# Kernel optimization log

Measured on AMD Instinct MI355X. Metric: run time of the kernel, lower is better.

Reference implementation:

```python
import jax, jax.numpy as jnp
import numpy as np

N, OBS, H, M, L = 512, 32, 128, 128, 3


def _w(key, shape, fan_in):
    return jax.random.normal(key, shape, dtype=jnp.float32) / np.sqrt(fan_in)


def setup_inputs() -> dict:
    key = jax.random.key(0)
    ks = iter(jax.random.split(key, 64))
    inp = {}
    inp["obs"] = jax.random.normal(next(ks), (N, OBS), dtype=jnp.float32)
    inp["pos"] = jax.random.uniform(next(ks), (N, 2), dtype=jnp.float32)
    # encoder: obs_dim -> H -> H -> H
    inp["enc_W1"] = _w(next(ks), (H, OBS), OBS); inp["enc_b1"] = jnp.zeros((H,), jnp.float32)
    inp["enc_W2"] = _w(next(ks), (H, H), H);     inp["enc_b2"] = jnp.zeros((H,), jnp.float32)
    inp["enc_W3"] = _w(next(ks), (H, H), H);     inp["enc_b3"] = jnp.zeros((H,), jnp.float32)
    # per-layer message MLPs: (2H+1) -> M -> M -> M, stacked over L layers
    inp["msg_W1"] = _w(next(ks), (L, M, 2 * H + 1), 2 * H + 1); inp["msg_b1"] = jnp.zeros((L, M), jnp.float32)
    inp["msg_W2"] = _w(next(ks), (L, M, M), M);                 inp["msg_b2"] = jnp.zeros((L, M), jnp.float32)
    inp["msg_W3"] = _w(next(ks), (L, M, M), M);                 inp["msg_b3"] = jnp.zeros((L, M), jnp.float32)
    # per-layer update MLPs: (H+M) -> H -> H -> H, stacked over L layers
    inp["upd_W1"] = _w(next(ks), (L, H, H + M), H + M); inp["upd_b1"] = jnp.zeros((L, H), jnp.float32)
    inp["upd_W2"] = _w(next(ks), (L, H, H), H);         inp["upd_b2"] = jnp.zeros((L, H), jnp.float32)
    inp["upd_W3"] = _w(next(ks), (L, H, H), H);         inp["upd_b3"] = jnp.zeros((L, H), jnp.float32)
    return inp


def _mlp3(x, W1, b1, W2, b2, W3, b3):
    h = jax.nn.relu(x @ W1.T + b1)
    h = jax.nn.relu(h @ W2.T + b2)
    return h @ W3.T + b3


def reference(obs, pos, enc_W1, enc_b1, enc_W2, enc_b2, enc_W3, enc_b3,
              msg_W1, msg_b1, msg_W2, msg_b2, msg_W3, msg_b3,
              upd_W1, upd_b1, upd_W2, upd_b2, upd_W3, upd_b3):
    n = obs.shape[0]
    h = enc_W1.shape[0]
    z = _mlp3(obs, enc_W1, enc_b1, enc_W2, enc_b2, enc_W3, enc_b3)  # (N, H)
    # pairwise distances; guard diagonal sqrt(0) for grad safety, then zero it
    diff = pos[:, None, :] - pos[None, :, :]                  # (N, N, 2)
    sq = jnp.sum(diff * diff, axis=-1)                        # (N, N)
    eye = jnp.eye(n, dtype=pos.dtype)
    dist = jnp.sqrt(jnp.where(eye > 0, 1.0, sq)) * (1.0 - eye)
    nondiag = (1.0 - eye)[:, :, None]
    n_layers = msg_W1.shape[0]
    for l in range(n_layers):
        W1 = msg_W1[l]
        Wi, Wj, wd = W1[:, :h], W1[:, h:2 * h], W1[:, 2 * h]  # split concat [z_i, z_j, d]
        A = z @ Wi.T                                          # (N, M) receiver term
        B = z @ Wj.T                                          # (N, M) sender term
        h1 = jax.nn.relu(A[:, None, :] + B[None, :, :] + dist[:, :, None] * wd + msg_b1[l])  # (N, N, M)
        h2 = jax.nn.relu(jnp.einsum('ijm,km->ijk', h1, msg_W2[l]) + msg_b2[l])
        m = jnp.einsum('ijm,km->ijk', h2, msg_W3[l]) + msg_b3[l]
        m = m * nondiag                                       # exclude j == i
        msum = jnp.sum(m, axis=1)                             # (N, M) sum over senders j
        z = _mlp3(jnp.concatenate([z, msum], axis=-1),
                  upd_W1[l], upd_b1[l], upd_W2[l], upd_b2[l], upd_W3[l], upd_b3[l])
    return z
```

## Files before the change

kernel.cpp:

```cpp
#include <hip/hip_runtime.h>

#define NA 512
#define NOBS 32
#define NH 128

typedef const float* fp32p;
typedef __attribute__((ext_vector_type(8))) short bf16x8;
typedef __attribute__((ext_vector_type(4))) float f32x4;

__device__ __forceinline__ unsigned cvt_pk_bf16(float lo, float hi) {
    unsigned r;
    asm("v_cvt_pk_bf16_f32 %0, %1, %2" : "=v"(r) : "v"(lo), "v"(hi));
    return r;
}

__device__ __forceinline__ bf16x8 wfrag_f4(const float* p) {
    float4 u = *(const float4*)p;
    float4 v = *(const float4*)(p + 4);
    union { unsigned w[4]; bf16x8 f; } r;
    r.w[0] = cvt_pk_bf16(u.x, u.y);
    r.w[1] = cvt_pk_bf16(u.z, u.w);
    r.w[2] = cvt_pk_bf16(v.x, v.y);
    r.w[3] = cvt_pk_bf16(v.z, v.w);
    return r.f;
}

__device__ __forceinline__ bf16x8 wfrag_s(const float* p) {
    union { unsigned w[4]; bf16x8 f; } r;
    r.w[0] = cvt_pk_bf16(p[0], p[1]);
    r.w[1] = cvt_pk_bf16(p[2], p[3]);
    r.w[2] = cvt_pk_bf16(p[4], p[5]);
    r.w[3] = cvt_pk_bf16(p[6], p[7]);
    return r.f;
}

#define HSTR 136

__global__ __launch_bounds__(512) void enc_ab_kernel(
    fp32p obs, fp32p eW1, fp32p eb1, fp32p eW2, fp32p eb2, fp32p eW3, fp32p eb3,
    fp32p mW1, float* __restrict__ z, float* __restrict__ A, float* __restrict__ B) {
    const int i0 = blockIdx.x * 16;
    const int t = threadIdx.x;
    const int lane = t & 63;
    const int w = t >> 6;
    const int q = lane >> 4;
    const int c = lane & 15;
    const int q8 = q * 8;
    const int ncol = w * 16 + c;

    __shared__ short ha[16 * HSTR];
    __shared__ short hb[16 * HSTR];

    {
        const bf16x8 af = wfrag_f4(obs + (size_t)(i0 + c) * NOBS + q8);
        const bf16x8 bf = wfrag_f4(eW1 + (size_t)ncol * NOBS + q8);
        f32x4 acc = {0.f, 0.f, 0.f, 0.f};
        acc = __builtin_amdgcn_mfma_f32_16x16x32_bf16(af, bf, acc, 0, 0, 0);
        const float bn = eb1[ncol];
        #pragma unroll
        for (int r = 0; r < 4; ++r) {
            const float v = fmaxf(acc[r] + bn, 0.f);
            ha[(q * 4 + r) * HSTR + ncol] = (short)cvt_pk_bf16(v, v);
        }
    }
    __syncthreads();
    {
        f32x4 acc = {0.f, 0.f, 0.f, 0.f};
        const short* ar = &ha[c * HSTR + q8];
        #pragma unroll
        for (int kb = 0; kb < 4; ++kb) {
            const bf16x8 a = *(const bf16x8*)(ar + kb * 32);
            const bf16x8 b = wfrag_f4(eW2 + (size_t)ncol * NH + kb * 32 + q8);
            acc = __builtin_amdgcn_mfma_f32_16x16x32_bf16(a, b, acc, 0, 0, 0);
        }
        const float bn = eb2[ncol];
        #pragma unroll
        for (int r = 0; r < 4; ++r) {
            const float v = fmaxf(acc[r] + bn, 0.f);
            hb[(q * 4 + r) * HSTR + ncol] = (short)cvt_pk_bf16(v, v);
        }
    }
    __syncthreads();
    {
        f32x4 acc = {0.f, 0.f, 0.f, 0.f};
        const short* ar = &hb[c * HSTR + q8];
        #pragma unroll
        for (int kb = 0; kb < 4; ++kb) {
            const bf16x8 a = *(const bf16x8*)(ar + kb * 32);
            const bf16x8 b = wfrag_f4(eW3 + (size_t)ncol * NH + kb * 32 + q8);
            acc = __builtin_amdgcn_mfma_f32_16x16x32_bf16(a, b, acc, 0, 0, 0);
        }
        const float bn = eb3[ncol];
        #pragma unroll
        for (int r = 0; r < 4; ++r) {
            const float v = acc[r] + bn;
            z[(size_t)(i0 + q * 4 + r) * NH + ncol] = v;
            ha[(q * 4 + r) * HSTR + ncol] = (short)cvt_pk_bf16(v, v);
        }
    }
    __syncthreads();
    {
        f32x4 aa = {0.f, 0.f, 0.f, 0.f};
        f32x4 ab = {0.f, 0.f, 0.f, 0.f};
        const short* ar = &ha[c * HSTR + q8];
        const float* wrow = mW1 + (size_t)ncol * 257;
        #pragma unroll
        for (int kb = 0; kb < 4; ++kb) {
            const bf16x8 a = *(const bf16x8*)(ar + kb * 32);
            const bf16x8 bi = wfrag_s(wrow + kb * 32 + q8);
            const bf16x8 bj = wfrag_s(wrow + 128 + kb * 32 + q8);
            aa = __builtin_amdgcn_mfma_f32_16x16x32_bf16(a, bi, aa, 0, 0, 0);
            ab = __builtin_amdgcn_mfma_f32_16x16x32_bf16(a, bj, ab, 0, 0, 0);
        }
        #pragma unroll
        for (int r = 0; r < 4; ++r) {
            A[(size_t)(i0 + q * 4 + r) * NH + ncol] = aa[r];
            B[(size_t)(i0 + q * 4 + r) * NH + ncol] = ab[r];
        }
    }
}

__global__ __launch_bounds__(512) void msg_upd_kernel(
    const float* __restrict__ A, const float* __restrict__ B,
    fp32p pos, const float* __restrict__ zin,
    fp32p W1l, fp32p b1, fp32p W2, fp32p b2, fp32p W3, fp32p b3,
    fp32p uW1, fp32p ub1, fp32p uW2, fp32p ub2, fp32p uW3, fp32p ub3,
    fp32p msgW1n, int do_ab,
    float* __restrict__ zout, float* __restrict__ An, float* __restrict__ Bn) {
    const int i = blockIdx.x;
    const int t = threadIdx.x;
    const int lane = t & 63;
    const int w = t >> 6;
    const int q = lane >> 4;
    const int c = lane & 15;
    const int ncol = w * 16 + c;

    __shared__ short h1s[128 * HSTR];
    __shared__ short h2s[128 * HSTR];
    __shared__ float distrow[NA];
    __shared__ float amrow[NH];
    __shared__ float wdsr[NH];
    __shared__ float xs2[2 * NH];
    __shared__ float part[4 * NH];
    __shared__ float part2[4 * NH];
    __shared__ float hx[NH], hy[NH], hz[NH];

    if (t < NH) {
        amrow[t] = A[i * NH + t] + b1[t];
        wdsr[t]  = W1l[t * 257 + 256];
        xs2[t] = zin[(size_t)i * NH + t];
    }
    {
        const float2 pi = *(const float2*)&pos[2 * i];
        const float2 pj = *(const float2*)&pos[2 * t];
        const float dx = pi.x - pj.x, dy = pi.y - pj.y;
        const float s = dx * dx + dy * dy;
        distrow[t] = (t == i) ? 0.0f : sqrtf(s);
    }

    bf16x8 w2f[4], w3f[4];
    {
        const float* w2r = W2 + (size_t)ncol * NH + q * 8;
        const float* w3r = W3 + (size_t)ncol * NH + q * 8;
        #pragma unroll
        for (int kb = 0; kb < 4; ++kb) {
            w2f[kb] = wfrag_f4(w2r + kb * 32);
            w3f[kb] = wfrag_f4(w3r + kb * 32);
        }
    }
    const float b2n = b2[ncol];

    const int m2 = lane * 2;
    float psum = 0.0f;

    __syncthreads();
    const float am0 = amrow[m2], am1 = amrow[m2 + 1];
    const float wd0 = wdsr[m2],  wd1 = wdsr[m2 + 1];

#define BUILD(c4_) do {                                                      \
        const int j0_ = (c4_) * 128;                                         \
        _Pragma("unroll")                                                    \
        for (int rr = 0; rr < 16; ++rr) {                                    \
            const int row_ = rr * 8 + w;                                     \
            const int jg_ = j0_ + row_;                                      \
            const float2 bv_ = *(const float2*)&B[(size_t)jg_ * NH + m2];    \
            const float d_ = distrow[jg_];                                   \
            const float v0_ = fmaxf(fmaf(d_, wd0, am0 + bv_.x), 0.0f);       \
            const float v1_ = fmaxf(fmaf(d_, wd1, am1 + bv_.y), 0.0f);       \
            *(unsigned*)&h1s[row_ * HSTR + m2] = cvt_pk_bf16(v0_, v1_);      \
        }                                                                    \
    } while (0)

#define GEMM1() do {                                                         \
        _Pragma("unroll")                                                    \
        for (int jt = 0; jt < 8; ++jt) {                                     \
            f32x4 acc = {0.f, 0.f, 0.f, 0.f};                                \
            const short* arow = &h1s[(jt * 16 + c) * HSTR + q * 8];          \
            _Pragma("unroll")                                                \
            for (int kb = 0; kb < 4; ++kb) {                                 \
                bf16x8 a = *(const bf16x8*)(arow + kb * 32);                 \
                acc = __builtin_amdgcn_mfma_f32_16x16x32_bf16(a, w2f[kb], acc, 0, 0, 0); \
            }                                                                \
            const int orow = jt * 16 + q * 4;                                \
            const unsigned p01 = cvt_pk_bf16(fmaxf(acc[0] + b2n, 0.0f),      \
                                             fmaxf(acc[1] + b2n, 0.0f));     \
            const unsigned p23 = cvt_pk_bf16(fmaxf(acc[2] + b2n, 0.0f),      \
                                             fmaxf(acc[3] + b2n, 0.0f));     \
            const unsigned send = (c & 1) ? p01 : p23;                       \
            const unsigned recv = __shfl_xor(send, 1, 64);                   \
            const unsigned keep = (c & 1) ? p23 : p01;                       \
            const unsigned lo = (c & 1) ? recv : keep;                       \
            const unsigned hi = (c & 1) ? keep : recv;                       \
            const unsigned d0 = (lo & 0xFFFFu) | (hi << 16);                 \
            const unsigned d1 = (lo >> 16) | (hi & 0xFFFF0000u);             \
            const int rbase = orow + ((c & 1) << 1);                         \
            const int colb = ncol & ~1;                                      \
            *(unsigned*)&h2s[(rbase + 0) * HSTR + colb] = d0;                \
            *(unsigned*)&h2s[(rbase + 1) * HSTR + colb] = d1;                \
        }                                                                    \
    } while (0)

#define GEMM2(c4_) do {                                                      \
        const int j0_ = (c4_) * 128;                                         \
        _Pragma("unroll")                                                    \
        for (int jt = 0; jt < 8; ++jt) {                                     \
            f32x4 acc = {0.f, 0.f, 0.f, 0.f};                                \
            const short* arow = &h2s[(jt * 16 + c) * HSTR + q * 8];          \
            _Pragma("unroll")                                                \
            for (int kb = 0; kb < 4; ++kb) {                                 \
                bf16x8 a = *(const bf16x8*)(arow + kb * 32);                 \
                acc = __builtin_amdgcn_mfma_f32_16x16x32_bf16(a, w3f[kb], acc, 0, 0, 0); \
            }                                                                \
            _Pragma("unroll")                                                \
            for (int r = 0; r < 4; ++r) {                                    \
                const int jg_ = j0_ + jt * 16 + q * 4 + r;                   \
                if (jg_ != i) psum += acc[r];                                \
            }                                                                \
        }                                                                    \
    } while (0)

    BUILD(0);
    __syncthreads();
    GEMM1();
    for (int c4 = 0; c4 < 4; ++c4) {
        __syncthreads();
        if (c4 < 3) {
            BUILD(c4 + 1);
            GEMM2(c4);
            __syncthreads();
            GEMM1();
        } else {
            GEMM2(c4);
        }
    }
#undef BUILD
#undef GEMM1
#undef GEMM2

    psum += __shfl_xor(psum, 16, 64);
    psum += __shfl_xor(psum, 32, 64);
    if (lane < 16) xs2[NH + ncol] = psum + 511.0f * b3[ncol];
    __syncthreads();

    const int nn = t >> 2;
    const int ks = t & 3;
    {
        const float* wr = uW1 + (size_t)nn * 256 + ks * 4;
        float p = 0.f;
        #pragma unroll
        for (int it = 0; it < 16; ++it) {
            const float4 wv = *(const float4*)(wr + it * 16);
            const float4 xv = *(const float4*)&xs2[it * 16 + ks * 4];
            p += wv.x * xv.x + wv.y * xv.y + wv.z * xv.z + wv.w * xv.w;
        }
        part[ks * NH + nn] = p;
    }
    __syncthreads();
    if (t < NH)
        hx[t] = fmaxf(ub1[t] + part[t] + part[NH + t] + part[2 * NH + t] + part[3 * NH + t], 0.f);
    __syncthreads();
    {
        const float* wr = uW2 + (size_t)nn * NH + ks * 4;
        float p = 0.f;
        #pragma unroll
        for (int it = 0; it < 8; ++it) {
            const float4 wv = *(const float4*)(wr + it * 16);
            const float4 xv = *(const float4*)&hx[it * 16 + ks * 4];
            p += wv.x * xv.x + wv.y * xv.y + wv.z * xv.z + wv.w * xv.w;
        }
        part[ks * NH + nn] = p;
    }
    __syncthreads();
    if (t < NH)
        hy[t] = fmaxf(ub2[t] + part[t] + part[NH + t] + part[2 * NH + t] + part[3 * NH + t], 0.f);
    __syncthreads();
    {
        const float* wr = uW3 + (size_t)nn * NH + ks * 4;
        float p = 0.f;
        #pragma unroll
        for (int it = 0; it < 8; ++it) {
            const float4 wv = *(const float4*)(wr + it * 16);
            const float4 xv = *(const float4*)&hy[it * 16 + ks * 4];
            p += wv.x * xv.x + wv.y * xv.y + wv.z * xv.z + wv.w * xv.w;
        }
        part[ks * NH + nn] = p;
    }
    __syncthreads();
    if (t < NH) {
        const float v = ub3[t] + part[t] + part[NH + t] + part[2 * NH + t] + part[3 * NH + t];
        zout[(size_t)i * NH + t] = v;
        hz[t] = v;
    }
    if (!do_ab) return;
    __syncthreads();
    {
        const float* pr = msgW1n + (size_t)nn * 257;
        float pa = 0.f, pb = 0.f;
        #pragma unroll
        for (int it = 0; it < 8; ++it) {
            #pragma unroll
            for (int j = 0; j < 4; ++j) {
                const int k = it * 16 + ks * 4 + j;
                const float x = hz[k];
                pa += x * pr[k];
                pb += x * pr[NH + k];
            }
        }
        part[ks * NH + nn] = pa;
        part2[ks * NH + nn] = pb;
    }
    __syncthreads();
    if (t < NH) {
        An[(size_t)i * NH + t] = part[t] + part[NH + t] + part[2 * NH + t] + part[3 * NH + t];
        Bn[(size_t)i * NH + t] = part2[t] + part2[NH + t] + part2[2 * NH + t] + part2[3 * NH + t];
    }
}

extern "C" void kernel_launch(void* const* d_in, const int* in_sizes, int n_in,
                              void* d_out, int out_size, void* d_ws, size_t ws_size,
                              hipStream_t stream) {
    fp32p obs   = (fp32p)d_in[0];
    fp32p pos   = (fp32p)d_in[1];
    fp32p encW1 = (fp32p)d_in[2];  fp32p encb1 = (fp32p)d_in[3];
    fp32p encW2 = (fp32p)d_in[4];  fp32p encb2 = (fp32p)d_in[5];
    fp32p encW3 = (fp32p)d_in[6];  fp32p encb3 = (fp32p)d_in[7];
    fp32p msgW1 = (fp32p)d_in[8];  fp32p msgb1 = (fp32p)d_in[9];
    fp32p msgW2 = (fp32p)d_in[10]; fp32p msgb2 = (fp32p)d_in[11];
    fp32p msgW3 = (fp32p)d_in[12]; fp32p msgb3 = (fp32p)d_in[13];
    fp32p updW1 = (fp32p)d_in[14]; fp32p updb1 = (fp32p)d_in[15];
    fp32p updW2 = (fp32p)d_in[16]; fp32p updb2 = (fp32p)d_in[17];
    fp32p updW3 = (fp32p)d_in[18]; fp32p updb3 = (fp32p)d_in[19];

    float* ws = (float*)d_ws;
    float* zA = ws;
    float* zB = zA + NA * NH;
    float* A0 = zB + NA * NH;
    float* B0 = A0 + NA * NH;
    float* A1 = B0 + NA * NH;
    float* B1 = A1 + NA * NH;

    enc_ab_kernel<<<NA / 16, 512, 0, stream>>>(obs, encW1, encb1, encW2, encb2,
                                               encW3, encb3, msgW1, zA, A0, B0);

    float* zin = zA;  float* zout = zB;
    float* Ac = A0;   float* Bc = B0;
    float* An = A1;   float* Bn = B1;
    for (int l = 0; l < 3; ++l) {
        const int do_ab = (l < 2);
        float* dst = (l == 2) ? (float*)d_out : zout;
        msg_upd_kernel<<<NA, 512, 0, stream>>>(Ac, Bc, pos, zin,
            msgW1 + (size_t)l * 128 * 257, msgb1 + l * 128,
            msgW2 + (size_t)l * 128 * 128, msgb2 + l * 128,
            msgW3 + (size_t)l * 128 * 128, msgb3 + l * 128,
            updW1 + (size_t)l * 256 * 128, updb1 + l * 128,
            updW2 + (size_t)l * 128 * 128, updb2 + l * 128,
            updW3 + (size_t)l * 128 * 128, updb3 + l * 128,
            msgW1 + (size_t)(l + 1 < 3 ? l + 1 : 0) * 128 * 257, do_ab,
            dst, An, Bn);
        float* tmp;
        tmp = zin; zin = zout; zout = tmp;
        tmp = Ac; Ac = An; An = tmp;
        tmp = Bc; Bc = Bn; Bn = tmp;
    }
}
```

Before: 207.8 us.

## Double-buffer 64-row message tiles and prefetch B rows into registers

Splits the per-receiver sender loop into eight 64-row chunks with double-buffered h1/h2 shared tiles. Global B loads for the next chunk are issued into registers before the current GEMM1, then converted and stored afterwards, so load latency overlaps with MFMA work. This also cuts barriers to one per iteration instead of two. In exchange it adds register pressure from the prefetched values and uses smaller MFMA batches per stage.

```diff
diff --git a/kernel.cpp b/kernel.cpp
--- a/kernel.cpp
+++ b/kernel.cpp
@@ -135,8 +135,8 @@
     const int c = lane & 15;
     const int ncol = w * 16 + c;
 
-    __shared__ short h1s[128 * HSTR];
-    __shared__ short h2s[128 * HSTR];
+    __shared__ short h1s[2][64 * HSTR];
+    __shared__ short h2s[2][64 * HSTR];
     __shared__ float distrow[NA];
     __shared__ float amrow[NH];
     __shared__ float wdsr[NH];
@@ -177,25 +177,37 @@
     const float am0 = amrow[m2], am1 = amrow[m2 + 1];
     const float wd0 = wdsr[m2],  wd1 = wdsr[m2 + 1];
 
-#define BUILD(c4_) do {                                                      \
-        const int j0_ = (c4_) * 128;                                         \
+    float2 bv[8];
+
+#define BLOAD(k_) do {                                                       \
+        const int j0_ = (k_) * 64;                                           \
         _Pragma("unroll")                                                    \
-        for (int rr = 0; rr < 16; ++rr) {                                    \
-            const int row_ = rr * 8 + w;                                     \
-            const int jg_ = j0_ + row_;                                      \
-            const float2 bv_ = *(const float2*)&B[(size_t)jg_ * NH + m2];    \
-            const float d_ = distrow[jg_];                                   \
-            const float v0_ = fmaxf(fmaf(d_, wd0, am0 + bv_.x), 0.0f);       \
-            const float v1_ = fmaxf(fmaf(d_, wd1, am1 + bv_.y), 0.0f);       \
-            *(unsigned*)&h1s[row_ * HSTR + m2] = cvt_pk_bf16(v0_, v1_);      \
+        for (int rr = 0; rr < 8; ++rr) {                                     \
+            const int jg_ = j0_ + rr * 8 + w;                                \
+            bv[rr] = *(const float2*)&B[(size_t)jg_ * NH + m2];              \
         }                                                                    \
     } while (0)
 
-#define GEMM1() do {                                                         \
+#define BSTORE(k_) do {                                                      \
+        const int j0_ = (k_) * 64;                                           \
+        short* h1d = h1s[(k_) & 1];                                          \
         _Pragma("unroll")                                                    \
-        for (int jt = 0; jt < 8; ++jt) {                                     \
+        for (int rr = 0; rr < 8; ++rr) {                                     \
+            const int row_ = rr * 8 + w;                                     \
+            const float d_ = distrow[j0_ + row_];                            \
+            const float v0_ = fmaxf(fmaf(d_, wd0, am0 + bv[rr].x), 0.0f);    \
+            const float v1_ = fmaxf(fmaf(d_, wd1, am1 + bv[rr].y), 0.0f);    \
+            *(unsigned*)&h1d[row_ * HSTR + m2] = cvt_pk_bf16(v0_, v1_);      \
+        }                                                                    \
+    } while (0)
+
+#define GEMM1(k_) do {                                                       \
+        const short* h1r = h1s[(k_) & 1];                                    \
+        short* h2d = h2s[(k_) & 1];                                          \
+        _Pragma("unroll")                                                    \
+        for (int jt = 0; jt < 4; ++jt) {                                     \
             f32x4 acc = {0.f, 0.f, 0.f, 0.f};                                \
-            const short* arow = &h1s[(jt * 16 + c) * HSTR + q * 8];          \
+            const short* arow = &h1r[(jt * 16 + c) * HSTR + q * 8];          \
             _Pragma("unroll")                                                \
             for (int kb = 0; kb < 4; ++kb) {                                 \
                 bf16x8 a = *(const bf16x8*)(arow + kb * 32);                 \
@@ -215,17 +227,18 @@
             const unsigned d1 = (lo >> 16) | (hi & 0xFFFF0000u);             \
             const int rbase = orow + ((c & 1) << 1);                         \
             const int colb = ncol & ~1;                                      \
-            *(unsigned*)&h2s[(rbase + 0) * HSTR + colb] = d0;                \
-            *(unsigned*)&h2s[(rbase + 1) * HSTR + colb] = d1;                \
+            *(unsigned*)&h2d[(rbase + 0) * HSTR + colb] = d0;                \
+            *(unsigned*)&h2d[(rbase + 1) * HSTR + colb] = d1;                \
         }                                                                    \
     } while (0)
 
-#define GEMM2(c4_) do {                                                      \
-        const int j0_ = (c4_) * 128;                                         \
+#define GEMM2(k_) do {                                                       \
+        const int j0_ = (k_) * 64;                                           \
+        const short* h2r = h2s[(k_) & 1];                                    \
         _Pragma("unroll")                                                    \
-        for (int jt = 0; jt < 8; ++jt) {                                     \
+        for (int jt = 0; jt < 4; ++jt) {                                     \
             f32x4 acc = {0.f, 0.f, 0.f, 0.f};                                \
-            const short* arow = &h2s[(jt * 16 + c) * HSTR + q * 8];          \
+            const short* arow = &h2r[(jt * 16 + c) * HSTR + q * 8];          \
             _Pragma("unroll")                                                \
             for (int kb = 0; kb < 4; ++kb) {                                 \
                 bf16x8 a = *(const bf16x8*)(arow + kb * 32);                 \
@@ -239,21 +252,21 @@
         }                                                                    \
     } while (0)
 
-    BUILD(0);
-    __syncthreads();
-    GEMM1();
-    for (int c4 = 0; c4 < 4; ++c4) {
+    BLOAD(0); BSTORE(0);
+    __syncthreads();
+    BLOAD(1); GEMM1(0); BSTORE(1);
+    __syncthreads();
+    #pragma unroll
+    for (int k = 1; k < 8; ++k) {
+        if (k < 7) BLOAD(k + 1);
+        GEMM1(k);
+        if (k < 7) BSTORE(k + 1);
+        GEMM2(k - 1);
         __syncthreads();
-        if (c4 < 3) {
-            BUILD(c4 + 1);
-            GEMM2(c4);
-            __syncthreads();
-            GEMM1();
-        } else {
-            GEMM2(c4);
-        }
-    }
-#undef BUILD
+    }
+    GEMM2(7);
+#undef BLOAD
+#undef BSTORE
 #undef GEMM1
 #undef GEMM2
 
```

New measurement: 207.8 us (median of 2 runs). Within noise of the previous version (+0.0%).
